# Kernel optimization log

Hardware: AMD Instinct MI355X
Metric: run time of the kernel (lower is better)

Reference implementation:

```python
import jax, jax.numpy as jnp
import numpy as np
from jax import lax

CIN, COUT, K, PAD = 256, 128, 3, 1


def setup_inputs() -> dict:
    key = jax.random.key(0)
    ks = jax.random.split(key, 5)
    N, h0, w0 = 2, 64, 64
    x = jax.random.normal(ks[0], (N, CIN, h0, w0), jnp.float32)
    lateral_feat = jax.random.normal(ks[1], (N, COUT, 1, 1), jnp.float32)
    trans_w = jax.random.normal(ks[2], (CIN, COUT, K, K), jnp.float32) * 0.02
    off_w1 = jax.random.normal(ks[3], (64, COUT, 3, 3), jnp.float32) * 0.02
    off_b1 = jnp.zeros((64,), jnp.float32)
    off_w2 = jax.random.normal(ks[4], (2 * K * K, 64, 3, 3), jnp.float32) * 0.02
    off_b2 = jnp.zeros((2 * K * K,), jnp.float32)
    return dict(x=x, lateral_feat=lateral_feat, trans_w=trans_w,
                off_w1=off_w1, off_b1=off_b1, off_w2=off_w2, off_b2=off_b2)


def _conv2d(x, w, b, pad):
    y = lax.conv_general_dilated(x, w, (1, 1), [(pad, pad), (pad, pad)],
                                 dimension_numbers=('NCHW', 'OIHW', 'NCHW'))
    return y + b[None, :, None, None]


def _conv_transpose2d(x, w, stride, pad, out_pad):
    # torch ConvTranspose2d weight layout: [Cin, Cout, k, k]
    k = w.shape[2]
    wt = jnp.flip(w, (2, 3)).transpose(1, 0, 2, 3)  # [Cout, Cin, k, k]
    lo = k - 1 - pad
    hi = k - 1 - pad + out_pad
    return lax.conv_general_dilated(x, wt, (1, 1), [(lo, hi), (lo, hi)],
                                    lhs_dilation=(stride, stride),
                                    dimension_numbers=('NCHW', 'OIHW', 'NCHW'))


def _deform_conv2d(x, offset, w, pad):
    # x [N,C,H,W], offset [N,2*K*K,H,W] (y,x interleaved per kernel tap), w [O,C,K,K]
    N, C, H, W = x.shape
    O = w.shape[0]
    KK = K * K
    off = offset.reshape(N, KK, 2, H, W)
    ky = jnp.arange(KK) // K
    kx = jnp.arange(KK) % K
    py = jnp.arange(H)[None, None, :, None] + (ky - pad)[None, :, None, None] + off[:, :, 0]
    px = jnp.arange(W)[None, None, None, :] + (kx - pad)[None, :, None, None] + off[:, :, 1]
    y0 = jnp.floor(py)
    x0 = jnp.floor(px)
    dy = py - y0
    dx = px - x0
    y0i = y0.astype(jnp.int32)
    x0i = x0.astype(jnp.int32)
    xf = x.reshape(N, C, H * W)

    def corner(yi, xi, wgt):
        valid = (yi >= 0) & (yi < H) & (xi >= 0) & (xi < W)
        idx = (jnp.clip(yi, 0, H - 1) * W + jnp.clip(xi, 0, W - 1)).reshape(N, -1)
        v = jnp.take_along_axis(xf, idx[:, None, :], axis=2).reshape(N, C, KK, H, W)
        return v * (wgt * valid)[:, None]

    sampled = (corner(y0i, x0i, (1 - dy) * (1 - dx))
               + corner(y0i, x0i + 1, (1 - dy) * dx)
               + corner(y0i + 1, x0i, dy * (1 - dx))
               + corner(y0i + 1, x0i + 1, dy * dx))  # [N,C,KK,H,W]
    return jnp.einsum('nckhw,ock->nohw', sampled, w.reshape(O, C, KK))


def reference(x, lateral_feat, trans_w, off_w1, off_b1, off_w2, off_b2):
    up = _conv_transpose2d(x, trans_w, 2, PAD, 1)          # [N, COUT, 2h0, 2w0]
    h = jax.nn.relu(_conv2d(lateral_feat, off_w1, off_b1, 1))
    offset = jnp.tanh(_conv2d(h, off_w2, off_b2, 1))       # [N, 18, 1, 1]
    N, C, H, W = up.shape
    # offset.repeat(1, 1, H, W) with 1x1 spatial input == broadcast to full grid
    offset = jnp.broadcast_to(offset, (N, 2 * K * K, H, W))
    # deform_conv2d uses trans_conv weight [O=CIN, I=COUT, K, K], stride=1, pad=PAD
    return _deform_conv2d(up, offset, trans_w, PAD)        # [N, CIN, H, W]
```

## Files before the change

### kernel.cpp

```cpp
#include <hip/hip_runtime.h>
#include <hip/hip_bf16.h>
#include <math.h>

#define CIN 256
#define COUT 128
#define NB 2

typedef __attribute__((ext_vector_type(8))) short s16x8;
typedef __attribute__((ext_vector_type(4))) float f32x4;

__device__ __forceinline__ unsigned short f2bf(float f) {
    union { float f; unsigned int u; } v; v.f = f;
    unsigned int u = v.u + 0x7FFFu + ((v.u >> 16) & 1u);
    return (unsigned short)(u >> 16);
}
__device__ __forceinline__ unsigned pk2(float lo, float hi) {
    __hip_bfloat162 h = __float22bfloat162_rn(make_float2(lo, hi));
    union { __hip_bfloat162 h; unsigned u; } v; v.h = h;
    return v.u;
}
__device__ __forceinline__ float blo(unsigned u) {
    union { unsigned u; float f; } v; v.u = u << 16; return v.f;
}
__device__ __forceinline__ float bhi(unsigned u) {
    union { unsigned u; float f; } v; v.u = u & 0xffff0000u; return v.f;
}

__global__ __launch_bounds__(256) void k_offset(const float* __restrict__ lat,
                         const float* __restrict__ w1, const float* __restrict__ b1,
                         const float* __restrict__ w2, const float* __restrict__ b2,
                         int* __restrict__ ipar, float* __restrict__ fpar) {
    __shared__ float w1c[64][129];
    __shared__ float h[NB][64];
    __shared__ float offv[NB][18];
    int t = threadIdx.x;
    for (int i = t; i < 8192; i += 256) w1c[i >> 7][i & 127] = w1[i * 9 + 4];
    __syncthreads();
    if (t < NB * 64) {
        int n = t >> 6, o = t & 63;
        float s = b1[o];
        const float* ln = lat + n * COUT;
#pragma unroll 8
        for (int c = 0; c < COUT; ++c) s += ln[c] * w1c[o][c];
        h[n][o] = fmaxf(s, 0.f);
    }
    __syncthreads();
    if (t < NB * 18) {
        int n = t / 18, j = t % 18;
        float s = b2[j];
        for (int o = 0; o < 64; ++o) s += h[n][o] * w2[(j * 64 + o) * 9 + 4];
        float ov = tanhf(s);
        ov = fminf(fmaxf(ov, -0.999999f), 0.999999f);
        offv[n][j] = ov;
    }
    __syncthreads();
    if (t < NB * 18) {
        int n = t / 18, j = t % 18;
        int tap = j >> 1, d = j & 1;
        float ov = offv[n][j];
        float fl = floorf(ov);
        int kc = d ? (tap % 3) : (tap / 3);
        ipar[(n * 9 + tap) * 2 + d] = kc - 1 + (int)fl;
        fpar[(n * 9 + tap) * 2 + d] = ov - fl;
    }
}

__global__ void k_prep_w(const float* __restrict__ tw,
                         unsigned short* __restrict__ A2,
                         unsigned short* __restrict__ Aw) {
    int i = blockIdx.x * 256 + threadIdx.x;
    const int NA = 256 * 1152;
    if (i < NA) {
        int o = i / 1152, k = i - o * 1152;
        int tap = k >> 7, c = k & 127;
        A2[i] = f2bf(tw[(o * 128 + c) * 9 + tap]);
    } else {
        int j = i - NA;
        if (j < 128 * 2304) {
            int co = j / 2304, k = j - co * 2304;
            int t9 = k >> 8, ci = k & 255;
            int ky = t9 / 3, kx = t9 - ky * 3;
            Aw[j] = f2bf(tw[(ci * 128 + co) * 9 + (2 - ky) * 3 + (2 - kx)]);
        }
    }
}

__global__ __launch_bounds__(256) void k_prep_x(const float* __restrict__ x,
                                                unsigned short* __restrict__ xp) {
    __shared__ float T[64][65];
    int t = threadIdx.x;
    int h = blockIdx.x;
    int c0 = blockIdx.y * 64;
    int n = blockIdx.z;
    {
        int wcol = t & 63, sub = t >> 6;
        for (int r = 0; r < 16; ++r) {
            int ci_l = r * 4 + sub;
            T[ci_l][wcol] = x[((n * 256 + c0 + ci_l) * 64 + h) * 64 + wcol];
        }
    }
    __syncthreads();
    int wcol = t >> 2, cg = t & 3;
    unsigned short* dst = xp + (size_t)n * (65 * 65 * 256) + (h * 65 + wcol) * 256 + c0 + cg * 16;
    unsigned pk[8];
#pragma unroll
    for (int j = 0; j < 8; ++j)
        pk[j] = pk2(T[cg * 16 + 2 * j][wcol], T[cg * 16 + 2 * j + 1][wcol]);
    *(uint4*)dst = make_uint4(pk[0], pk[1], pk[2], pk[3]);
    *(uint4*)(dst + 8) = make_uint4(pk[4], pk[5], pk[6], pk[7]);
}

__global__ __launch_bounds__(256) void k_tconv2(const unsigned short* __restrict__ xp,
                                                const unsigned short* __restrict__ Aw,
                                                unsigned short* __restrict__ upp) {
    __shared__ unsigned short As[128][40];
    __shared__ unsigned short Bs[64][40];
    int t = threadIdx.x;
    int b = blockIdx.x;
    int phase = b >> 8, j = b & 255;
    int n = j >> 7, xpar = ((j >> 6) & 1) ^ phase, yh = j & 63;
    int y = yh * 2 + phase;
    const unsigned short* xpn = xp + (size_t)n * (65 * 65 * 256);

    int lane = t & 63, w = t >> 6;
    int col = lane & 15, q = lane >> 4;
    int wm = w >> 1, wn = w & 1;
    int bx = t >> 2, bcg = t & 3;

    f32x4 acc[4][2];
#pragma unroll
    for (int mi = 0; mi < 4; ++mi)
#pragma unroll
        for (int ni = 0; ni < 2; ++ni) acc[mi][ni] = (f32x4){0.f, 0.f, 0.f, 0.f};

    int kys[2], kxs[2], nky, nkx;
    if (phase) { kys[0] = 0; kys[1] = 2; nky = 2; } else { kys[0] = 1; nky = 1; }
    if (xpar)  { kxs[0] = 0; kxs[1] = 2; nkx = 2; } else { kxs[0] = 1; nkx = 1; }

    for (int a1 = 0; a1 < nky; ++a1) {
        int ky = kys[a1];
        int d2 = (y + ky - 1) >> 1;
        for (int a2 = 0; a2 < nkx; ++a2) {
            int kx = kxs[a2];
            int s = (xpar + kx - 1) >> 1;
            const unsigned short* brow = xpn + ((d2 * 65) + s + bx) * 256 + bcg * 8;
            int t9 = ky * 3 + kx;
            for (int cb = 0; cb < 256; cb += 32) {
                __syncthreads();
#pragma unroll
                for (int it = 0; it < 2; ++it) {
                    int gid = it * 256 + t;
                    int row = gid >> 2, cg = gid & 3;
                    *(uint4*)&As[row][cg * 8] = *(const uint4*)(Aw + row * 2304 + t9 * 256 + cb + cg * 8);
                }
                *(uint4*)&Bs[bx][bcg * 8] = *(const uint4*)(brow + cb);
                __syncthreads();
                s16x8 a[4], bb[2];
#pragma unroll
                for (int mi = 0; mi < 4; ++mi)
                    a[mi] = *(const s16x8*)&As[wm * 64 + mi * 16 + col][q * 8];
#pragma unroll
                for (int ni = 0; ni < 2; ++ni)
                    bb[ni] = *(const s16x8*)&Bs[wn * 32 + ni * 16 + col][q * 8];
#pragma unroll
                for (int mi = 0; mi < 4; ++mi)
#pragma unroll
                    for (int ni = 0; ni < 2; ++ni)
                        acc[mi][ni] = __builtin_amdgcn_mfma_f32_16x16x32_bf16(a[mi], bb[ni], acc[mi][ni], 0, 0, 0);
            }
        }
    }
    unsigned short* uppn = upp + (size_t)n * (132 * 132 * 128);
#pragma unroll
    for (int mi = 0; mi < 4; ++mi)
#pragma unroll
        for (int ni = 0; ni < 2; ++ni) {
            int co = wm * 64 + mi * 16 + q * 4;
            int p64 = wn * 32 + ni * 16 + col;
            int xg = 2 * p64 + xpar;
            unsigned short* p = uppn + ((y + 2) * 132 + (xg + 2)) * 128 + co;
            unsigned lo = pk2(acc[mi][ni][0], acc[mi][ni][1]);
            unsigned hi = pk2(acc[mi][ni][2], acc[mi][ni][3]);
            *(uint2*)p = make_uint2(lo, hi);
        }
}

__global__ __launch_bounds__(256) void k_deform2(const unsigned short* __restrict__ upp,
                                                 const unsigned short* __restrict__ A2,
                                                 const int* __restrict__ ipar,
                                                 const float* __restrict__ fpar,
                                                 float* __restrict__ out) {
    __shared__ unsigned short As[256][40];
    __shared__ unsigned short Bs[64][40];
    int t = threadIdx.x;
    int b = blockIdx.x;
    int xcd = b & 7, j = b >> 3;
    int n = xcd >> 2, band = xcd & 3;
    int y = band * 32 + (j & 31);
    int tx0 = (j >> 5) * 64;
    const unsigned short* uppn = upp + (size_t)n * (132 * 132 * 128);

    int lane = t & 63, w = t >> 6;
    int col = lane & 15, q = lane >> 4;
    int bx = t >> 2, bcg = t & 3;

    int iyA[9], ixA[9];
    float w00[9], w01[9], w10[9], w11[9];
#pragma unroll
    for (int tap = 0; tap < 9; ++tap) {
        iyA[tap] = ipar[(n * 9 + tap) * 2 + 0];
        ixA[tap] = ipar[(n * 9 + tap) * 2 + 1];
        float fy = fpar[(n * 9 + tap) * 2 + 0];
        float fx = fpar[(n * 9 + tap) * 2 + 1];
        w00[tap] = (1.f - fy) * (1.f - fx);
        w01[tap] = (1.f - fy) * fx;
        w10[tap] = fy * (1.f - fx);
        w11[tap] = fy * fx;
    }

    f32x4 acc[4][4];
#pragma unroll
    for (int mi = 0; mi < 4; ++mi)
#pragma unroll
        for (int ni = 0; ni < 4; ++ni) acc[mi][ni] = (f32x4){0.f, 0.f, 0.f, 0.f};

    for (int tap = 0; tap < 9; ++tap) {
        int y2 = y + 2 + iyA[tap];
        const unsigned short* rowp = uppn + ((y2 * 132) + (tx0 + 2 + ixA[tap] + bx)) * 128 + bcg * 8;
        float c00 = w00[tap], c01 = w01[tap], c10 = w10[tap], c11 = w11[tap];
        for (int cb = 0; cb < 128; cb += 32) {
            __syncthreads();
            int kb = tap * 128 + cb;
#pragma unroll
            for (int it = 0; it < 4; ++it) {
                int gid = it * 256 + t;
                int row = gid >> 2, cg = gid & 3;
                *(uint4*)&As[row][cg * 8] = *(const uint4*)(A2 + row * 1152 + kb + cg * 8);
            }
            {
                const unsigned short* p = rowp + cb;
                uint4 uA = *(const uint4*)p;
                uint4 uB = *(const uint4*)(p + 128);
                uint4 uC = *(const uint4*)(p + 16896);
                uint4 uD = *(const uint4*)(p + 17024);
                unsigned ua[4] = {uA.x, uA.y, uA.z, uA.w};
                unsigned ub[4] = {uB.x, uB.y, uB.z, uB.w};
                unsigned uc[4] = {uC.x, uC.y, uC.z, uC.w};
                unsigned ud[4] = {uD.x, uD.y, uD.z, uD.w};
                unsigned pk[4];
#pragma unroll
                for (int i = 0; i < 4; ++i) {
                    float vL = c00 * blo(ua[i]) + c01 * blo(ub[i]) + c10 * blo(uc[i]) + c11 * blo(ud[i]);
                    float vH = c00 * bhi(ua[i]) + c01 * bhi(ub[i]) + c10 * bhi(uc[i]) + c11 * bhi(ud[i]);
                    pk[i] = pk2(vL, vH);
                }
                *(uint4*)&Bs[bx][bcg * 8] = make_uint4(pk[0], pk[1], pk[2], pk[3]);
            }
            __syncthreads();
            s16x8 a[4], bb[4];
#pragma unroll
            for (int mi = 0; mi < 4; ++mi)
                a[mi] = *(const s16x8*)&As[w * 64 + mi * 16 + col][q * 8];
#pragma unroll
            for (int ni = 0; ni < 4; ++ni)
                bb[ni] = *(const s16x8*)&Bs[ni * 16 + col][q * 8];
#pragma unroll
            for (int mi = 0; mi < 4; ++mi)
#pragma unroll
                for (int ni = 0; ni < 4; ++ni)
                    acc[mi][ni] = __builtin_amdgcn_mfma_f32_16x16x32_bf16(a[mi], bb[ni], acc[mi][ni], 0, 0, 0);
        }
    }
#pragma unroll
    for (int mi = 0; mi < 4; ++mi)
#pragma unroll
        for (int ni = 0; ni < 4; ++ni) {
            int o = w * 64 + mi * 16 + q * 4;
            int xg = tx0 + ni * 16 + col;
            float* p = out + (((size_t)(n * 256 + o)) * 128 + y) * 128 + xg;
            p[0]         = acc[mi][ni][0];
            p[16384]     = acc[mi][ni][1];
            p[2 * 16384] = acc[mi][ni][2];
            p[3 * 16384] = acc[mi][ni][3];
        }
}

extern "C" void kernel_launch(void* const* d_in, const int* in_sizes, int n_in,
                              void* d_out, int out_size, void* d_ws, size_t ws_size,
                              hipStream_t stream) {
    const float* x   = (const float*)d_in[0];
    const float* lat = (const float*)d_in[1];
    const float* tw  = (const float*)d_in[2];
    const float* w1  = (const float*)d_in[3];
    const float* b1  = (const float*)d_in[4];
    const float* w2  = (const float*)d_in[5];
    const float* b2  = (const float*)d_in[6];
    float* out = (float*)d_out;

    char* ws = (char*)d_ws;
    unsigned short* upp = (unsigned short*)ws;
    unsigned short* xp  = (unsigned short*)(ws + 8921088);
    unsigned short* A2  = (unsigned short*)(ws + 13247488);
    unsigned short* Aw  = (unsigned short*)(ws + 13837312);
    int*   ipar         = (int*)(ws + 14427136);
    float* fpar         = (float*)(ws + 14427280);

    hipMemsetAsync(upp, 0, 8921088, stream);
    hipMemsetAsync(xp, 0, 4326400, stream);

    k_offset<<<1, 256, 0, stream>>>(lat, w1, b1, w2, b2, ipar, fpar);
    k_prep_w<<<2304, 256, 0, stream>>>(tw, A2, Aw);
    k_prep_x<<<dim3(64, 4, 2), 256, 0, stream>>>(x, xp);
    k_tconv2<<<512, 256, 0, stream>>>(xp, Aw, upp);
    k_deform2<<<512, 256, 0, stream>>>(upp, A2, ipar, fpar, out);
}
```

Measured before the change: 160.9 us.

## Fuse prep kernels, pre-swizzle weights into MFMA fragment order, double-buffer GEMM loops

Merges the offset, weight-prep and input-transpose kernels into one launch and folds the two memsets into one. Weights are written in a per-lane MFMA fragment layout, so both GEMM kernels load A operands straight from global memory into registers instead of staging them through LDS. The B tile is double-buffered in LDS and the next tile's loads are issued before the current MFMAs, leaving one barrier per step instead of two. The aim is to cut launch overhead, LDS traffic and sync stalls, at the cost of more register use and A loads that are no longer shared through LDS.

```diff
diff --git a/kernel.cpp b/kernel.cpp
--- a/kernel.cpp
+++ b/kernel.cpp
@@ -1,10 +1,6 @@
 #include <hip/hip_runtime.h>
 #include <hip/hip_bf16.h>
 #include <math.h>
-
-#define CIN 256
-#define COUT 128
-#define NB 2
 
 typedef __attribute__((ext_vector_type(8))) short s16x8;
 typedef __attribute__((ext_vector_type(4))) float f32x4;
@@ -26,99 +22,140 @@
     union { unsigned u; float f; } v; v.u = u & 0xffff0000u; return v.f;
 }
 
-__global__ __launch_bounds__(256) void k_offset(const float* __restrict__ lat,
-                         const float* __restrict__ w1, const float* __restrict__ b1,
-                         const float* __restrict__ w2, const float* __restrict__ b2,
-                         int* __restrict__ ipar, float* __restrict__ fpar) {
-    __shared__ float w1c[64][129];
-    __shared__ float h[NB][64];
-    __shared__ float offv[NB][18];
-    int t = threadIdx.x;
-    for (int i = t; i < 8192; i += 256) w1c[i >> 7][i & 127] = w1[i * 9 + 4];
-    __syncthreads();
-    if (t < NB * 64) {
-        int n = t >> 6, o = t & 63;
-        float s = b1[o];
-        const float* ln = lat + n * COUT;
+__device__ __forceinline__ void blend_store(uint4 uA, uint4 uB, uint4 uC, uint4 uD,
+                                            float4 cw, unsigned short* dst) {
+    unsigned ua[4] = {uA.x, uA.y, uA.z, uA.w};
+    unsigned ub[4] = {uB.x, uB.y, uB.z, uB.w};
+    unsigned uc[4] = {uC.x, uC.y, uC.z, uC.w};
+    unsigned ud[4] = {uD.x, uD.y, uD.z, uD.w};
+    unsigned pk[4];
+#pragma unroll
+    for (int i = 0; i < 4; ++i) {
+        float vL = cw.x * blo(ua[i]) + cw.y * blo(ub[i]) + cw.z * blo(uc[i]) + cw.w * blo(ud[i]);
+        float vH = cw.x * bhi(ua[i]) + cw.y * bhi(ub[i]) + cw.z * bhi(uc[i]) + cw.w * bhi(ud[i]);
+        pk[i] = pk2(vL, vH);
+    }
+    *(uint4*)dst = make_uint4(pk[0], pk[1], pk[2], pk[3]);
+}
+
+__global__ __launch_bounds__(256) void k_prep(const float* __restrict__ x,
+                                              const float* __restrict__ lat,
+                                              const float* __restrict__ tw,
+                                              const float* __restrict__ w1,
+                                              const float* __restrict__ b1,
+                                              const float* __restrict__ w2,
+                                              const float* __restrict__ b2,
+                                              unsigned short* __restrict__ xp,
+                                              unsigned short* __restrict__ A2f,
+                                              unsigned short* __restrict__ Awf,
+                                              int* __restrict__ ipar,
+                                              float* __restrict__ fpar) {
+    __shared__ float sm[8420];
+    int b = blockIdx.x, t = threadIdx.x;
+    if (b == 0) {
+        for (int i = t; i < 8192; i += 256) sm[(i >> 7) * 129 + (i & 127)] = w1[i * 9 + 4];
+        __syncthreads();
+        if (t < 128) {
+            int n = t >> 6, o = t & 63;
+            float s = b1[o];
+            const float* ln = lat + n * 128;
 #pragma unroll 8
-        for (int c = 0; c < COUT; ++c) s += ln[c] * w1c[o][c];
-        h[n][o] = fmaxf(s, 0.f);
-    }
-    __syncthreads();
-    if (t < NB * 18) {
-        int n = t / 18, j = t % 18;
-        float s = b2[j];
-        for (int o = 0; o < 64; ++o) s += h[n][o] * w2[(j * 64 + o) * 9 + 4];
-        float ov = tanhf(s);
-        ov = fminf(fmaxf(ov, -0.999999f), 0.999999f);
-        offv[n][j] = ov;
-    }
-    __syncthreads();
-    if (t < NB * 18) {
-        int n = t / 18, j = t % 18;
-        int tap = j >> 1, d = j & 1;
-        float ov = offv[n][j];
-        float fl = floorf(ov);
-        int kc = d ? (tap % 3) : (tap / 3);
-        ipar[(n * 9 + tap) * 2 + d] = kc - 1 + (int)fl;
-        fpar[(n * 9 + tap) * 2 + d] = ov - fl;
-    }
-}
-
-__global__ void k_prep_w(const float* __restrict__ tw,
-                         unsigned short* __restrict__ A2,
-                         unsigned short* __restrict__ Aw) {
-    int i = blockIdx.x * 256 + threadIdx.x;
-    const int NA = 256 * 1152;
-    if (i < NA) {
-        int o = i / 1152, k = i - o * 1152;
-        int tap = k >> 7, c = k & 127;
-        A2[i] = f2bf(tw[(o * 128 + c) * 9 + tap]);
+            for (int c = 0; c < 128; ++c) s += ln[c] * sm[o * 129 + c];
+            sm[8256 + t] = fmaxf(s, 0.f);
+        }
+        __syncthreads();
+        if (t < 36) {
+            int n = t / 18, j = t % 18;
+            float s = b2[j];
+            for (int o = 0; o < 64; ++o) s += sm[8256 + n * 64 + o] * w2[(j * 64 + o) * 9 + 4];
+            float ov = tanhf(s);
+            ov = fminf(fmaxf(ov, -0.999999f), 0.999999f);
+            sm[8384 + t] = ov;
+        }
+        __syncthreads();
+        if (t < 36) {
+            int n = t / 18, j = t % 18;
+            int tap = j >> 1, d = j & 1;
+            float ov = sm[8384 + t];
+            float fl = floorf(ov);
+            int kc = d ? (tap % 3) : (tap / 3);
+            ipar[(n * 9 + tap) * 2 + d] = kc - 1 + (int)fl;
+            fpar[(n * 9 + tap) * 2 + d] = ov - fl;
+        }
+    } else if (b < 145) {
+        int slot = (b - 1) * 256 + t;
+        int l = slot & 63;
+        int mi = (slot >> 6) & 3;
+        int w = (slot >> 8) & 3;
+        int k = slot >> 10;
+        int row = w * 64 + mi * 16 + (l & 15);
+        int kq = l >> 4;
+        unsigned short v[8];
+#pragma unroll
+        for (int j = 0; j < 8; ++j) {
+            int kcol = k * 32 + kq * 8 + j;
+            int tap = kcol >> 7, c = kcol & 127;
+            v[j] = f2bf(tw[(row * 128 + c) * 9 + tap]);
+        }
+        unsigned p0 = (unsigned)v[0] | ((unsigned)v[1] << 16);
+        unsigned p1 = (unsigned)v[2] | ((unsigned)v[3] << 16);
+        unsigned p2 = (unsigned)v[4] | ((unsigned)v[5] << 16);
+        unsigned p3 = (unsigned)v[6] | ((unsigned)v[7] << 16);
+        *(uint4*)(A2f + slot * 8) = make_uint4(p0, p1, p2, p3);
+    } else if (b < 289) {
+        int slot = (b - 145) * 256 + t;
+        int l = slot & 63;
+        int mi = (slot >> 6) & 3;
+        int wm = (slot >> 8) & 1;
+        int k = slot >> 9;
+        int row = wm * 64 + mi * 16 + (l & 15);
+        int kq = l >> 4;
+        unsigned short v[8];
+#pragma unroll
+        for (int j = 0; j < 8; ++j) {
+            int kcol = k * 32 + kq * 8 + j;
+            int t9 = kcol >> 8, ci = kcol & 255;
+            int ky = t9 / 3, kx = t9 - ky * 3;
+            v[j] = f2bf(tw[(ci * 128 + row) * 9 + (2 - ky) * 3 + (2 - kx)]);
+        }
+        unsigned p0 = (unsigned)v[0] | ((unsigned)v[1] << 16);
+        unsigned p1 = (unsigned)v[2] | ((unsigned)v[3] << 16);
+        unsigned p2 = (unsigned)v[4] | ((unsigned)v[5] << 16);
+        unsigned p3 = (unsigned)v[6] | ((unsigned)v[7] << 16);
+        *(uint4*)(Awf + slot * 8) = make_uint4(p0, p1, p2, p3);
     } else {
-        int j = i - NA;
-        if (j < 128 * 2304) {
-            int co = j / 2304, k = j - co * 2304;
-            int t9 = k >> 8, ci = k & 255;
-            int ky = t9 / 3, kx = t9 - ky * 3;
-            Aw[j] = f2bf(tw[(ci * 128 + co) * 9 + (2 - ky) * 3 + (2 - kx)]);
-        }
-    }
-}
-
-__global__ __launch_bounds__(256) void k_prep_x(const float* __restrict__ x,
-                                                unsigned short* __restrict__ xp) {
-    __shared__ float T[64][65];
-    int t = threadIdx.x;
-    int h = blockIdx.x;
-    int c0 = blockIdx.y * 64;
-    int n = blockIdx.z;
-    {
-        int wcol = t & 63, sub = t >> 6;
-        for (int r = 0; r < 16; ++r) {
-            int ci_l = r * 4 + sub;
-            T[ci_l][wcol] = x[((n * 256 + c0 + ci_l) * 64 + h) * 64 + wcol];
-        }
-    }
-    __syncthreads();
-    int wcol = t >> 2, cg = t & 3;
-    unsigned short* dst = xp + (size_t)n * (65 * 65 * 256) + (h * 65 + wcol) * 256 + c0 + cg * 16;
-    unsigned pk[8];
-#pragma unroll
-    for (int j = 0; j < 8; ++j)
-        pk[j] = pk2(T[cg * 16 + 2 * j][wcol], T[cg * 16 + 2 * j + 1][wcol]);
-    *(uint4*)dst = make_uint4(pk[0], pk[1], pk[2], pk[3]);
-    *(uint4*)(dst + 8) = make_uint4(pk[4], pk[5], pk[6], pk[7]);
-}
-
-__global__ __launch_bounds__(256) void k_tconv2(const unsigned short* __restrict__ xp,
-                                                const unsigned short* __restrict__ Aw,
+        int bb = b - 289;
+        int h = bb & 63, cq = (bb >> 6) & 3, n = bb >> 8;
+        int c0 = cq * 64;
+        {
+            int wcol = t & 63, sub = t >> 6;
+            for (int r = 0; r < 16; ++r) {
+                int ci_l = r * 4 + sub;
+                sm[ci_l * 65 + wcol] = x[((n * 256 + c0 + ci_l) * 64 + h) * 64 + wcol];
+            }
+        }
+        __syncthreads();
+        int wcol = t >> 2, cg = t & 3;
+        unsigned short* dst = xp + (size_t)n * (65 * 65 * 256) + (h * 65 + wcol) * 256 + c0 + cg * 16;
+        unsigned pk[8];
+#pragma unroll
+        for (int j = 0; j < 8; ++j)
+            pk[j] = pk2(sm[(cg * 16 + 2 * j) * 65 + wcol], sm[(cg * 16 + 2 * j + 1) * 65 + wcol]);
+        *(uint4*)dst = make_uint4(pk[0], pk[1], pk[2], pk[3]);
+        *(uint4*)(dst + 8) = make_uint4(pk[4], pk[5], pk[6], pk[7]);
+    }
+}
+
+__global__ __launch_bounds__(256) void k_tconv3(const unsigned short* __restrict__ xp,
+                                                const unsigned short* __restrict__ Awf,
                                                 unsigned short* __restrict__ upp) {
-    __shared__ unsigned short As[128][40];
-    __shared__ unsigned short Bs[64][40];
+    __shared__ unsigned short Bs[2][64][40];
+    __shared__ int st9[4];
+    __shared__ int sbb[4];
     int t = threadIdx.x;
     int b = blockIdx.x;
-    int phase = b >> 8, j = b & 255;
-    int n = j >> 7, xpar = ((j >> 6) & 1) ^ phase, yh = j & 63;
+    int phase = b >> 8, jj = b & 255;
+    int n = jj >> 7, xpar = ((jj >> 6) & 1) ^ phase, yh = jj & 63;
     int y = yh * 2 + phase;
     const unsigned short* xpn = xp + (size_t)n * (65 * 65 * 256);
 
@@ -126,6 +163,21 @@
     int col = lane & 15, q = lane >> 4;
     int wm = w >> 1, wn = w & 1;
     int bx = t >> 2, bcg = t & 3;
+    int boff = bx * 256 + bcg * 8;
+
+    int kys[2], kxs[2], nky, nkx;
+    if (phase) { kys[0] = 0; kys[1] = 2; nky = 2; } else { kys[0] = 1; kys[1] = 1; nky = 1; }
+    if (xpar)  { kxs[0] = 0; kxs[1] = 2; nkx = 2; } else { kxs[0] = 1; kxs[1] = 1; nkx = 1; }
+    int nslots = nky * nkx;
+    if (t < nslots) {
+        int a1 = t / nkx, a2 = t % nkx;
+        int ky = kys[a1], kx = kxs[a2];
+        st9[t] = ky * 3 + kx;
+        int d2 = (y + ky - 1) >> 1;
+        int s = (xpar + kx - 1) >> 1;
+        sbb[t] = (d2 * 65 + s) * 256;
+    }
+    int NT = nslots * 8;
 
     f32x4 acc[4][2];
 #pragma unroll
@@ -133,43 +185,51 @@
 #pragma unroll
         for (int ni = 0; ni < 2; ++ni) acc[mi][ni] = (f32x4){0.f, 0.f, 0.f, 0.f};
 
-    int kys[2], kxs[2], nky, nkx;
-    if (phase) { kys[0] = 0; kys[1] = 2; nky = 2; } else { kys[0] = 1; nky = 1; }
-    if (xpar)  { kxs[0] = 0; kxs[1] = 2; nkx = 2; } else { kxs[0] = 1; nkx = 1; }
-
-    for (int a1 = 0; a1 < nky; ++a1) {
-        int ky = kys[a1];
-        int d2 = (y + ky - 1) >> 1;
-        for (int a2 = 0; a2 < nkx; ++a2) {
-            int kx = kxs[a2];
-            int s = (xpar + kx - 1) >> 1;
-            const unsigned short* brow = xpn + ((d2 * 65) + s + bx) * 256 + bcg * 8;
-            int t9 = ky * 3 + kx;
-            for (int cb = 0; cb < 256; cb += 32) {
-                __syncthreads();
-#pragma unroll
-                for (int it = 0; it < 2; ++it) {
-                    int gid = it * 256 + t;
-                    int row = gid >> 2, cg = gid & 3;
-                    *(uint4*)&As[row][cg * 8] = *(const uint4*)(Aw + row * 2304 + t9 * 256 + cb + cg * 8);
-                }
-                *(uint4*)&Bs[bx][bcg * 8] = *(const uint4*)(brow + cb);
-                __syncthreads();
-                s16x8 a[4], bb[2];
-#pragma unroll
-                for (int mi = 0; mi < 4; ++mi)
-                    a[mi] = *(const s16x8*)&As[wm * 64 + mi * 16 + col][q * 8];
-#pragma unroll
-                for (int ni = 0; ni < 2; ++ni)
-                    bb[ni] = *(const s16x8*)&Bs[wn * 32 + ni * 16 + col][q * 8];
-#pragma unroll
-                for (int mi = 0; mi < 4; ++mi)
-#pragma unroll
-                    for (int ni = 0; ni < 2; ++ni)
-                        acc[mi][ni] = __builtin_amdgcn_mfma_f32_16x16x32_bf16(a[mi], bb[ni], acc[mi][ni], 0, 0, 0);
-            }
-        }
-    }
+    __syncthreads();
+
+    const unsigned short* Afw = Awf + wm * 2048 + lane * 8;
+    s16x8 a_cur[4], a_nxt[4];
+
+    {
+        int kAw0 = st9[0] * 8;
+        uint4 bv = *(const uint4*)(xpn + sbb[0] + boff);
+        *(uint4*)&Bs[0][bx][bcg * 8] = bv;
+#pragma unroll
+        for (int mi = 0; mi < 4; ++mi)
+            a_cur[mi] = *(const s16x8*)(Afw + kAw0 * 4096 + mi * 512);
+    }
+    __syncthreads();
+
+    for (int cc = 0; cc < NT; ++cc) {
+        int cc1 = cc + 1;
+        uint4 bv;
+        if (cc1 < NT) {
+            int slot1 = cc1 >> 3, cb1 = cc1 & 7;
+            int t9v = st9[slot1];
+            int base = sbb[slot1];
+            bv = *(const uint4*)(xpn + base + cb1 * 32 + boff);
+            int kAw1 = t9v * 8 + cb1;
+#pragma unroll
+            for (int mi = 0; mi < 4; ++mi)
+                a_nxt[mi] = *(const s16x8*)(Afw + kAw1 * 4096 + mi * 512);
+        }
+        s16x8 bb[2];
+#pragma unroll
+        for (int ni = 0; ni < 2; ++ni)
+            bb[ni] = *(const s16x8*)&Bs[cc & 1][wn * 32 + ni * 16 + col][q * 8];
+#pragma unroll
+        for (int mi = 0; mi < 4; ++mi)
+#pragma unroll
+            for (int ni = 0; ni < 2; ++ni)
+                acc[mi][ni] = __builtin_amdgcn_mfma_f32_16x16x32_bf16(a_cur[mi], bb[ni], acc[mi][ni], 0, 0, 0);
+        if (cc1 < NT) {
+            *(uint4*)&Bs[cc1 & 1][bx][bcg * 8] = bv;
+#pragma unroll
+            for (int mi = 0; mi < 4; ++mi) a_cur[mi] = a_nxt[mi];
+        }
+        __syncthreads();
+    }
+
     unsigned short* uppn = upp + (size_t)n * (132 * 132 * 128);
 #pragma unroll
     for (int mi = 0; mi < 4; ++mi)
@@ -185,13 +245,14 @@
         }
 }
 
-__global__ __launch_bounds__(256) void k_deform2(const unsigned short* __restrict__ upp,
-                                                 const unsigned short* __restrict__ A2,
+__global__ __launch_bounds__(256) void k_deform3(const unsigned short* __restrict__ upp,
+                                                 const unsigned short* __restrict__ A2f,
                                                  const int* __restrict__ ipar,
                                                  const float* __restrict__ fpar,
                                                  float* __restrict__ out) {
-    __shared__ unsigned short As[256][40];
-    __shared__ unsigned short Bs[64][40];
+    __shared__ unsigned short Bs[2][64][40];
+    __shared__ int sbase[9];
+    __shared__ float4 swt[9];
     int t = threadIdx.x;
     int b = blockIdx.x;
     int xcd = b & 7, j = b >> 3;
@@ -203,19 +264,13 @@
     int lane = t & 63, w = t >> 6;
     int col = lane & 15, q = lane >> 4;
     int bx = t >> 2, bcg = t & 3;
-
-    int iyA[9], ixA[9];
-    float w00[9], w01[9], w10[9], w11[9];
-#pragma unroll
-    for (int tap = 0; tap < 9; ++tap) {
-        iyA[tap] = ipar[(n * 9 + tap) * 2 + 0];
-        ixA[tap] = ipar[(n * 9 + tap) * 2 + 1];
-        float fy = fpar[(n * 9 + tap) * 2 + 0];
-        float fx = fpar[(n * 9 + tap) * 2 + 1];
-        w00[tap] = (1.f - fy) * (1.f - fx);
-        w01[tap] = (1.f - fy) * fx;
-        w10[tap] = fy * (1.f - fx);
-        w11[tap] = fy * fx;
+    int boff = bx * 128 + bcg * 8;
+
+    if (t < 9) {
+        int iy = ipar[(n * 9 + t) * 2 + 0], ix = ipar[(n * 9 + t) * 2 + 1];
+        float fy = fpar[(n * 9 + t) * 2 + 0], fx = fpar[(n * 9 + t) * 2 + 1];
+        sbase[t] = ((y + 2 + iy) * 132 + (tx0 + 2 + ix)) * 128;
+        swt[t] = make_float4((1.f - fy) * (1.f - fx), (1.f - fy) * fx, fy * (1.f - fx), fy * fx);
     }
 
     f32x4 acc[4][4];
@@ -224,53 +279,59 @@
 #pragma unroll
         for (int ni = 0; ni < 4; ++ni) acc[mi][ni] = (f32x4){0.f, 0.f, 0.f, 0.f};
 
-    for (int tap = 0; tap < 9; ++tap) {
-        int y2 = y + 2 + iyA[tap];
-        const unsigned short* rowp = uppn + ((y2 * 132) + (tx0 + 2 + ixA[tap] + bx)) * 128 + bcg * 8;
-        float c00 = w00[tap], c01 = w01[tap], c10 = w10[tap], c11 = w11[tap];
-        for (int cb = 0; cb < 128; cb += 32) {
-            __syncthreads();
-            int kb = tap * 128 + cb;
-#pragma unroll
-            for (int it = 0; it < 4; ++it) {
-                int gid = it * 256 + t;
-                int row = gid >> 2, cg = gid & 3;
-                *(uint4*)&As[row][cg * 8] = *(const uint4*)(A2 + row * 1152 + kb + cg * 8);
-            }
-            {
-                const unsigned short* p = rowp + cb;
-                uint4 uA = *(const uint4*)p;
-                uint4 uB = *(const uint4*)(p + 128);
-                uint4 uC = *(const uint4*)(p + 16896);
-                uint4 uD = *(const uint4*)(p + 17024);
-                unsigned ua[4] = {uA.x, uA.y, uA.z, uA.w};
-                unsigned ub[4] = {uB.x, uB.y, uB.z, uB.w};
-                unsigned uc[4] = {uC.x, uC.y, uC.z, uC.w};
-                unsigned ud[4] = {uD.x, uD.y, uD.z, uD.w};
-                unsigned pk[4];
-#pragma unroll
-                for (int i = 0; i < 4; ++i) {
-                    float vL = c00 * blo(ua[i]) + c01 * blo(ub[i]) + c10 * blo(uc[i]) + c11 * blo(ud[i]);
-                    float vH = c00 * bhi(ua[i]) + c01 * bhi(ub[i]) + c10 * bhi(uc[i]) + c11 * bhi(ud[i]);
-                    pk[i] = pk2(vL, vH);
-                }
-                *(uint4*)&Bs[bx][bcg * 8] = make_uint4(pk[0], pk[1], pk[2], pk[3]);
-            }
-            __syncthreads();
-            s16x8 a[4], bb[4];
+    __syncthreads();
+
+    const unsigned short* Afw = A2f + w * 2048 + lane * 8;
+    s16x8 a_cur[4], a_nxt[4];
+
+    {
+        const unsigned short* p = uppn + sbase[0] + boff;
+        uint4 uA = *(const uint4*)p;
+        uint4 uB = *(const uint4*)(p + 128);
+        uint4 uC = *(const uint4*)(p + 16896);
+        uint4 uD = *(const uint4*)(p + 17024);
+        blend_store(uA, uB, uC, uD, swt[0], &Bs[0][bx][bcg * 8]);
+#pragma unroll
+        for (int mi = 0; mi < 4; ++mi)
+            a_cur[mi] = *(const s16x8*)(Afw + mi * 512);
+    }
+    __syncthreads();
+
+#pragma unroll 2
+    for (int k = 0; k < 36; ++k) {
+        int k1 = k + 1;
+        uint4 uA, uB, uC, uD;
+        float4 cw;
+        if (k1 < 36) {
+            int t1 = k1 >> 2, cb1 = (k1 & 3) * 32;
+            int base = sbase[t1];
+            cw = swt[t1];
+            const unsigned short* p = uppn + base + cb1 + boff;
+            uA = *(const uint4*)p;
+            uB = *(const uint4*)(p + 128);
+            uC = *(const uint4*)(p + 16896);
+            uD = *(const uint4*)(p + 17024);
 #pragma unroll
             for (int mi = 0; mi < 4; ++mi)
-                a[mi] = *(const s16x8*)&As[w * 64 + mi * 16 + col][q * 8];
+                a_nxt[mi] = *(const s16x8*)(Afw + k1 * 8192 + mi * 512);
+        }
+        s16x8 bb[4];
+#pragma unroll
+        for (int ni = 0; ni < 4; ++ni)
+            bb[ni] = *(const s16x8*)&Bs[k & 1][ni * 16 + col][q * 8];
+#pragma unroll
+        for (int mi = 0; mi < 4; ++mi)
 #pragma unroll
             for (int ni = 0; ni < 4; ++ni)
-                bb[ni] = *(const s16x8*)&Bs[ni * 16 + col][q * 8];
-#pragma unroll
-            for (int mi = 0; mi < 4; ++mi)
-#pragma unroll
-                for (int ni = 0; ni < 4; ++ni)
-                    acc[mi][ni] = __builtin_amdgcn_mfma_f32_16x16x32_bf16(a[mi], bb[ni], acc[mi][ni], 0, 0, 0);
-        }
-    }
+                acc[mi][ni] = __builtin_amdgcn_mfma_f32_16x16x32_bf16(a_cur[mi], bb[ni], acc[mi][ni], 0, 0, 0);
+        if (k1 < 36) {
+            blend_store(uA, uB, uC, uD, cw, &Bs[k1 & 1][bx][bcg * 8]);
+#pragma unroll
+            for (int mi = 0; mi < 4; ++mi) a_cur[mi] = a_nxt[mi];
+        }
+        __syncthreads();
+    }
+
 #pragma unroll
     for (int mi = 0; mi < 4; ++mi)
 #pragma unroll
@@ -300,17 +361,13 @@
     char* ws = (char*)d_ws;
     unsigned short* upp = (unsigned short*)ws;
     unsigned short* xp  = (unsigned short*)(ws + 8921088);
-    unsigned short* A2  = (unsigned short*)(ws + 13247488);
-    unsigned short* Aw  = (unsigned short*)(ws + 13837312);
+    unsigned short* A2f = (unsigned short*)(ws + 13247488);
+    unsigned short* Awf = (unsigned short*)(ws + 13837312);
     int*   ipar         = (int*)(ws + 14427136);
-    float* fpar         = (float*)(ws + 14427280);
-
-    hipMemsetAsync(upp, 0, 8921088, stream);
-    hipMemsetAsync(xp, 0, 4326400, stream);
-
-    k_offset<<<1, 256, 0, stream>>>(lat, w1, b1, w2, b2, ipar, fpar);
-    k_prep_w<<<2304, 256, 0, stream>>>(tw, A2, Aw);
-    k_prep_x<<<dim3(64, 4, 2), 256, 0, stream>>>(x, xp);
-    k_tconv2<<<512, 256, 0, stream>>>(xp, Aw, upp);
-    k_deform2<<<512, 256, 0, stream>>>(upp, A2, ipar, fpar, out);
-}
+    float* fpar         = (float*)(ws + 14427424);
+
+    hipMemsetAsync(ws, 0, 13247488, stream);
+    k_prep<<<801, 256, 0, stream>>>(x, lat, tw, w1, b1, w2, b2, xp, A2f, Awf, ipar, fpar);
+    k_tconv3<<<512, 256, 0, stream>>>(xp, Awf, upp);
+    k_deform3<<<512, 256, 0, stream>>>(upp, A2f, ipar, fpar, out);
+}
```

Measured after the change: 150.4 us. 1.07x faster.
